# Kernel tuning notes

Measured on AMD Instinct MI355X. Metric: run time of the kernel, lower is better.

Reference implementation:

```python
import jax, jax.numpy as jnp
import numpy as np

_DN = ('NCHW', 'OIHW', 'NCHW')


def _gaussian_kernel1d(ksize, sigma):
    x = np.arange(ksize, dtype=np.float32) - ksize // 2
    g = np.exp(-x ** 2 / (2.0 * sigma ** 2))
    return (g / g.sum()).astype(np.float32)


def _nms_kernels():
    # kornia get_canny_nms_kernel: kernel k = center - neighbor at angle k*45deg (0deg = +x/right)
    k = np.zeros((8, 1, 3, 3), dtype=np.float32)
    offs = [(0, 1), (-1, 1), (-1, 0), (-1, -1), (0, -1), (1, -1), (1, 0), (1, 1)]
    for i, (dy, dx) in enumerate(offs):
        k[i, 0, 1, 1] = 1.0
        k[i, 0, 1 + dy, 1 + dx] = -1.0
    return k


def _conv(x, w, padding):
    return jax.lax.conv_general_dilated(x, w, (1, 1), padding, dimension_numbers=_DN)


def _canny_magnitude(data):
    eps = 1e-6
    x = (data + 1.0) / 2.0
    # rgb -> grayscale (kornia weights)
    rgb_w = jnp.array([0.299, 0.587, 0.114], dtype=x.dtype)
    gray = jnp.einsum('bchw,c->bhw', x, rgb_w)[:, None]  # [B,1,H,W]
    # gaussian blur 5x5, sigma=1, reflect border (kornia default), separable
    g1d = jnp.asarray(_gaussian_kernel1d(5, 1.0), dtype=x.dtype)
    p = jnp.pad(gray, ((0, 0), (0, 0), (2, 2), (2, 2)), mode='reflect')
    blurred = _conv(_conv(p, g1d.reshape(1, 1, 1, 5), 'VALID'), g1d.reshape(1, 1, 5, 1), 'VALID')
    # sobel spatial gradient (normalized=False), replicate padding
    sob_x = jnp.array([[-1., 0., 1.], [-2., 0., 2.], [-1., 0., 1.]], dtype=x.dtype)
    sob = jnp.stack([sob_x, sob_x.T])[:, None]  # [2,1,3,3]
    bp = jnp.pad(blurred, ((0, 0), (0, 0), (1, 1), (1, 1)), mode='edge')
    grads = _conv(bp, sob, 'VALID')  # [B,2,H,W]
    gx, gy = grads[:, 0:1], grads[:, 1:2]
    magnitude = jnp.sqrt(gx * gx + gy * gy + eps)  # [B,1,H,W]
    # angle rounded to nearest 45 degrees
    ang45 = jnp.round(jnp.rad2deg(jnp.arctan2(gy, gx)) / 45.0)
    # non-maximum suppression: center-minus-neighbor along 8 directions (zero pad)
    nms_k = jnp.asarray(_nms_kernels(), dtype=x.dtype)
    nms_mag = _conv(magnitude, nms_k, ((1, 1), (1, 1)))  # [B,8,H,W]
    idx_pos = ang45.astype(jnp.int32) % 8
    idx_neg = (idx_pos + 4) % 8
    sel_pos = jnp.take_along_axis(nms_mag, idx_pos, axis=1)
    sel_neg = jnp.take_along_axis(nms_mag, idx_neg, axis=1)
    is_max = jnp.minimum(sel_pos, sel_neg) > 0.0
    return magnitude * is_max


def setup_inputs() -> dict:
    key = jax.random.key(0)
    data = jax.random.normal(key, (16, 3, 512, 512), dtype=jnp.float32)
    return {'data': data}


def reference(data):
    # EdgeOperator.forward: canny((data+1)/2)[0] -> NMS'd gradient magnitude [B,1,H,W]
    return _canny_magnitude(data)
```

## Files before the change

### kernel.cpp

```cpp
#include <hip/hip_runtime.h>
#include <math.h>

#define IMH 512
#define IMW 512
#define T   32
#define GS  40

#define LG  44
#define OG  0
#define LH  40
#define OH  1760
#define LB  40
#define OB  3360
#define LM  40
#define OM  4800
#define LX  32
#define OGX 0
#define OGY 1024
#define NPOOL 6160

__device__ __forceinline__ int reflect_i(int v, int n) {
    if (v < 0) v = -v;
    if (v >= n) v = 2 * n - 2 - v;
    return v;
}
__device__ __forceinline__ int clamp_i(int v, int n) {
    return v < 0 ? 0 : (v >= n ? n - 1 : v);
}

__global__ __launch_bounds__(256)
void canny_mag_kernel(const float* __restrict__ data, float* __restrict__ out) {
    __shared__ __align__(16) float sP[NPOOL];
    const int bx0 = blockIdx.x * T;
    const int by0 = blockIdx.y * T;
    const int b   = blockIdx.z;
    const int tid = threadIdx.x;
    const bool xin = (bx0 >= 4) && (bx0 + T + 4 <= IMW);
    const bool bin = (bx0 >= 1) && (bx0 + T + 1 <= IMW) &&
                     (by0 >= 1) && (by0 + T + 1 <= IMH);

    const float w0 = 0.05448868f, w1 = 0.24420134f, w2 = 0.40261995f;
    const size_t plane = (size_t)IMH * IMW;
    const float* p0 = data + (size_t)b * 3 * plane;
    const float* p1 = p0 + plane;
    const float* p2 = p1 + plane;

    if (xin) {
        for (int idx = tid; idx < GS * 10; idx += 256) {
            int r = idx / 10, c4 = idx - r * 10;
            int ry = reflect_i(by0 - 4 + r, IMH);
            int off = ry * IMW + (bx0 - 4) + c4 * 4;
            const float4 a = *(const float4*)(p0 + off);
            const float4 g = *(const float4*)(p1 + off);
            const float4 c = *(const float4*)(p2 + off);
            float4 o;
            o.x = 0.1495f * a.x + 0.2935f * g.x + 0.057f * c.x + 0.5f;
            o.y = 0.1495f * a.y + 0.2935f * g.y + 0.057f * c.y + 0.5f;
            o.z = 0.1495f * a.z + 0.2935f * g.z + 0.057f * c.z + 0.5f;
            o.w = 0.1495f * a.w + 0.2935f * g.w + 0.057f * c.w + 0.5f;
            *(float4*)&sP[OG + r * LG + c4 * 4] = o;
        }
    } else {
        for (int idx = tid; idx < GS * GS; idx += 256) {
            int i = idx / GS, j = idx - i * GS;
            int ry = reflect_i(by0 - 4 + i, IMH);
            int rx = reflect_i(bx0 - 4 + j, IMW);
            int off = ry * IMW + rx;
            sP[OG + i * LG + j] = 0.1495f * p0[off] + 0.2935f * p1[off] + 0.057f * p2[off] + 0.5f;
        }
    }
    __syncthreads();

    if (xin) {
        for (int idx = tid; idx < GS * 9; idx += 256) {
            int i = idx / 9, gq = idx - i * 9;
            const float4 A = *(const float4*)&sP[OG + i * LG + 4 * gq];
            const float4 Bv = *(const float4*)&sP[OG + i * LG + 4 * gq + 4];
            float W0 = A.x, W1 = A.y, W2 = A.z, W3 = A.w;
            float W4 = Bv.x, W5 = Bv.y, W6 = Bv.z, W7 = Bv.w;
            float4 o;
            o.x = w0 * (W0 + W4) + w1 * (W1 + W3) + w2 * W2;
            o.y = w0 * (W1 + W5) + w1 * (W2 + W4) + w2 * W3;
            o.z = w0 * (W2 + W6) + w1 * (W3 + W5) + w2 * W4;
            o.w = w0 * (W3 + W7) + w1 * (W4 + W6) + w2 * W5;
            *(float4*)&sP[OH + i * LH + 4 * gq] = o;
        }
    } else {
        for (int idx = tid; idx < GS * 36; idx += 256) {
            int i = idx / 36, j = idx - i * 36;
            int cj = clamp_i(bx0 - 2 + j, IMW) - bx0 + 4;
            const float* gp = &sP[OG + i * LG + cj];
            sP[OH + i * LH + j] = w0 * (gp[-2] + gp[2]) + w1 * (gp[-1] + gp[1]) + w2 * gp[0];
        }
    }
    __syncthreads();

    for (int idx = tid; idx < 36 * 9; idx += 256) {
        int jy = idx / 9, gq = idx - jy * 9;
        int ci = clamp_i(by0 - 2 + jy, IMH) - by0 + 4;
        int base = OH + ci * LH + 4 * gq;
        const float4 r0 = *(const float4*)&sP[base - 2 * LH];
        const float4 r1 = *(const float4*)&sP[base - LH];
        const float4 r2 = *(const float4*)&sP[base];
        const float4 r3 = *(const float4*)&sP[base + LH];
        const float4 r4 = *(const float4*)&sP[base + 2 * LH];
        float4 o;
        o.x = w0 * (r0.x + r4.x) + w1 * (r1.x + r3.x) + w2 * r2.x;
        o.y = w0 * (r0.y + r4.y) + w1 * (r1.y + r3.y) + w2 * r2.y;
        o.z = w0 * (r0.z + r4.z) + w1 * (r1.z + r3.z) + w2 * r2.z;
        o.w = w0 * (r0.w + r4.w) + w1 * (r1.w + r3.w) + w2 * r2.w;
        *(float4*)&sP[OB + jy * LB + 4 * gq + 4] = o;
    }
    __syncthreads();

    for (int idx = tid; idx < 34 * 10; idx += 256) {
        int iy = idx / 10, gq = idx - iy * 10;
        int baseB = OB + iy * LB + 4 * gq;
        const float4 t0a = *(const float4*)&sP[baseB];
        const float4 t0b = *(const float4*)&sP[baseB + 4];
        const float4 t1a = *(const float4*)&sP[baseB + LB];
        const float4 t1b = *(const float4*)&sP[baseB + LB + 4];
        const float4 t2a = *(const float4*)&sP[baseB + 2 * LB];
        const float4 t2b = *(const float4*)&sP[baseB + 2 * LB + 4];
        float W0[8] = {t0a.x, t0a.y, t0a.z, t0a.w, t0b.x, t0b.y, t0b.z, t0b.w};
        float W1[8] = {t1a.x, t1a.y, t1a.z, t1a.w, t1b.x, t1b.y, t1b.z, t1b.w};
        float W2[8] = {t2a.x, t2a.y, t2a.z, t2a.w, t2b.x, t2b.y, t2b.z, t2b.w};
        float mg[4], gxv[4], gyv[4];
        #pragma unroll
        for (int k = 0; k < 4; ++k) {
            float a00 = W0[k + 1], a01 = W0[k + 2], a02 = W0[k + 3];
            float a10 = W1[k + 1],                  a12 = W1[k + 3];
            float a20 = W2[k + 1], a21 = W2[k + 2], a22 = W2[k + 3];
            float gx = (a02 - a00) + 2.0f * (a12 - a10) + (a22 - a20);
            float gy = (a20 - a00) + 2.0f * (a21 - a01) + (a22 - a02);
            float m = sqrtf(gx * gx + gy * gy + 1e-6f);
            if (!bin) {
                int my = by0 - 1 + iy;
                int cx = bx0 - 4 + 4 * gq + k;
                if (my < 0 || my >= IMH || cx < 0 || cx >= IMW) m = 0.0f;
            }
            mg[k] = m; gxv[k] = gx; gyv[k] = gy;
        }
        *(float4*)&sP[OM + iy * LM + 4 * gq] = make_float4(mg[0], mg[1], mg[2], mg[3]);
        if (gq >= 1 && gq <= 8 && iy >= 1 && iy <= 32) {
            int st = (iy - 1) * LX + 4 * gq - 4;
            *(float4*)&sP[OGX + st] = make_float4(gxv[0], gxv[1], gxv[2], gxv[3]);
            *(float4*)&sP[OGY + st] = make_float4(gyv[0], gyv[1], gyv[2], gyv[3]);
        }
    }
    __syncthreads();

    {
        const int ly  = tid >> 3;
        const int lx0 = (tid & 7) * 4;
        const float4 mag4 = *(const float4*)&sP[OM + (ly + 1) * LM + lx0 + 4];
        const float4 gx4  = *(const float4*)&sP[OGX + ly * LX + lx0];
        const float4 gy4  = *(const float4*)&sP[OGY + ly * LX + lx0];
        const float magv[4] = {mag4.x, mag4.y, mag4.z, mag4.w};
        const float gxv2[4] = {gx4.x, gx4.y, gx4.z, gx4.w};
        const float gyv2[4] = {gy4.x, gy4.y, gy4.z, gy4.w};
        float ov[4];
        #pragma unroll
        for (int k = 0; k < 4; ++k) {
            float gx = gxv2[k], gy = gyv2[k], mag = magv[k];
            float ax = fabsf(gx), ay = fabsf(gy);
            int dy, dx;
            if (ay <= 0.41421356237f * ax)      { dy = 0; dx = 1; }
            else if (ay >= 2.41421356237f * ax) { dy = 1; dx = 0; }
            else                                { dx = 1; dy = (gx * gy > 0.0f) ? -1 : 1; }
            float n1 = sP[OM + (ly + 1 + dy) * LM + (lx0 + k + 4 + dx)];
            float n2 = sP[OM + (ly + 1 - dy) * LM + (lx0 + k + 4 - dx)];
            ov[k] = (mag > n1 && mag > n2) ? mag : 0.0f;
        }
        float4 o4 = make_float4(ov[0], ov[1], ov[2], ov[3]);
        *(float4*)&out[(size_t)b * plane + (size_t)(by0 + ly) * IMW + (bx0 + lx0)] = o4;
    }
}

extern "C" void kernel_launch(void* const* d_in, const int* in_sizes, int n_in,
                              void* d_out, int out_size, void* d_ws, size_t ws_size,
                              hipStream_t stream) {
    const float* data = (const float*)d_in[0];
    float* out = (float*)d_out;
    int B = in_sizes[0] / (3 * IMH * IMW);
    dim3 grid(IMW / T, IMH / T, B);
    canny_mag_kernel<<<grid, dim3(256, 1, 1), 0, stream>>>(data, out);
}
```

Measured before the change: 104.5 us.

## Fuse grayscale with horizontal blur and alias shared buffers to cut LDS

```diff
diff --git a/kernel.cpp b/kernel.cpp
--- a/kernel.cpp
+++ b/kernel.cpp
@@ -4,20 +4,14 @@
 #define IMH 512
 #define IMW 512
 #define T   32
-#define GS  40
 
-#define LG  44
-#define OG  0
-#define LH  40
-#define OH  1760
+#define LH  36
+#define OH  0
+#define LM  40
+#define OM  0
 #define LB  40
-#define OB  3360
-#define LM  40
-#define OM  4800
-#define LX  32
-#define OGX 0
-#define OGY 1024
-#define NPOOL 6160
+#define OB  1440
+#define NPOOL 3200
 
 __device__ __forceinline__ int reflect_i(int v, int n) {
     if (v < 0) v = -v;
@@ -28,7 +22,7 @@
     return v < 0 ? 0 : (v >= n ? n - 1 : v);
 }
 
-__global__ __launch_bounds__(256)
+__global__ __launch_bounds__(256, 8)
 void canny_mag_kernel(const float* __restrict__ data, float* __restrict__ out) {
     __shared__ __align__(16) float sP[NPOOL];
     const int bx0 = blockIdx.x * T;
@@ -46,50 +40,45 @@
     const float* p2 = p1 + plane;
 
     if (xin) {
-        for (int idx = tid; idx < GS * 10; idx += 256) {
-            int r = idx / 10, c4 = idx - r * 10;
-            int ry = reflect_i(by0 - 4 + r, IMH);
-            int off = ry * IMW + (bx0 - 4) + c4 * 4;
-            const float4 a = *(const float4*)(p0 + off);
-            const float4 g = *(const float4*)(p1 + off);
-            const float4 c = *(const float4*)(p2 + off);
+        for (int idx = tid; idx < 40 * 9; idx += 256) {
+            int i = idx / 9, gq = idx - i * 9;
+            int ry = reflect_i(by0 - 4 + i, IMH);
+            int off = ry * IMW + (bx0 - 4) + 4 * gq;
+            const float4 a0 = *(const float4*)(p0 + off);
+            const float4 a1 = *(const float4*)(p0 + off + 4);
+            const float4 g0 = *(const float4*)(p1 + off);
+            const float4 g1 = *(const float4*)(p1 + off + 4);
+            const float4 c0 = *(const float4*)(p2 + off);
+            const float4 c1 = *(const float4*)(p2 + off + 4);
+            float w[8];
+            w[0] = 0.1495f * a0.x + 0.2935f * g0.x + 0.057f * c0.x + 0.5f;
+            w[1] = 0.1495f * a0.y + 0.2935f * g0.y + 0.057f * c0.y + 0.5f;
+            w[2] = 0.1495f * a0.z + 0.2935f * g0.z + 0.057f * c0.z + 0.5f;
+            w[3] = 0.1495f * a0.w + 0.2935f * g0.w + 0.057f * c0.w + 0.5f;
+            w[4] = 0.1495f * a1.x + 0.2935f * g1.x + 0.057f * c1.x + 0.5f;
+            w[5] = 0.1495f * a1.y + 0.2935f * g1.y + 0.057f * c1.y + 0.5f;
+            w[6] = 0.1495f * a1.z + 0.2935f * g1.z + 0.057f * c1.z + 0.5f;
+            w[7] = 0.1495f * a1.w + 0.2935f * g1.w + 0.057f * c1.w + 0.5f;
             float4 o;
-            o.x = 0.1495f * a.x + 0.2935f * g.x + 0.057f * c.x + 0.5f;
-            o.y = 0.1495f * a.y + 0.2935f * g.y + 0.057f * c.y + 0.5f;
-            o.z = 0.1495f * a.z + 0.2935f * g.z + 0.057f * c.z + 0.5f;
-            o.w = 0.1495f * a.w + 0.2935f * g.w + 0.057f * c.w + 0.5f;
-            *(float4*)&sP[OG + r * LG + c4 * 4] = o;
+            o.x = w0 * (w[0] + w[4]) + w1 * (w[1] + w[3]) + w2 * w[2];
+            o.y = w0 * (w[1] + w[5]) + w1 * (w[2] + w[4]) + w2 * w[3];
+            o.z = w0 * (w[2] + w[6]) + w1 * (w[3] + w[5]) + w2 * w[4];
+            o.w = w0 * (w[3] + w[7]) + w1 * (w[4] + w[6]) + w2 * w[5];
+            *(float4*)&sP[OH + i * LH + 4 * gq] = o;
         }
     } else {
-        for (int idx = tid; idx < GS * GS; idx += 256) {
-            int i = idx / GS, j = idx - i * GS;
+        for (int idx = tid; idx < 40 * 40; idx += 256) {
+            int i = idx / 40, j = idx - i * 40;
             int ry = reflect_i(by0 - 4 + i, IMH);
             int rx = reflect_i(bx0 - 4 + j, IMW);
             int off = ry * IMW + rx;
-            sP[OG + i * LG + j] = 0.1495f * p0[off] + 0.2935f * p1[off] + 0.057f * p2[off] + 0.5f;
+            sP[OB + i * 40 + j] = 0.1495f * p0[off] + 0.2935f * p1[off] + 0.057f * p2[off] + 0.5f;
         }
-    }
-    __syncthreads();
-
-    if (xin) {
-        for (int idx = tid; idx < GS * 9; idx += 256) {
-            int i = idx / 9, gq = idx - i * 9;
-            const float4 A = *(const float4*)&sP[OG + i * LG + 4 * gq];
-            const float4 Bv = *(const float4*)&sP[OG + i * LG + 4 * gq + 4];
-            float W0 = A.x, W1 = A.y, W2 = A.z, W3 = A.w;
-            float W4 = Bv.x, W5 = Bv.y, W6 = Bv.z, W7 = Bv.w;
-            float4 o;
-            o.x = w0 * (W0 + W4) + w1 * (W1 + W3) + w2 * W2;
-            o.y = w0 * (W1 + W5) + w1 * (W2 + W4) + w2 * W3;
-            o.z = w0 * (W2 + W6) + w1 * (W3 + W5) + w2 * W4;
-            o.w = w0 * (W3 + W7) + w1 * (W4 + W6) + w2 * W5;
-            *(float4*)&sP[OH + i * LH + 4 * gq] = o;
-        }
-    } else {
-        for (int idx = tid; idx < GS * 36; idx += 256) {
+        __syncthreads();
+        for (int idx = tid; idx < 40 * 36; idx += 256) {
             int i = idx / 36, j = idx - i * 36;
             int cj = clamp_i(bx0 - 2 + j, IMW) - bx0 + 4;
-            const float* gp = &sP[OG + i * LG + cj];
+            const float* gp = &sP[OB + i * 40 + cj];
             sP[OH + i * LH + j] = w0 * (gp[-2] + gp[2]) + w1 * (gp[-1] + gp[1]) + w2 * gp[0];
         }
     }
@@ -125,7 +114,7 @@
         float W0[8] = {t0a.x, t0a.y, t0a.z, t0a.w, t0b.x, t0b.y, t0b.z, t0b.w};
         float W1[8] = {t1a.x, t1a.y, t1a.z, t1a.w, t1b.x, t1b.y, t1b.z, t1b.w};
         float W2[8] = {t2a.x, t2a.y, t2a.z, t2a.w, t2b.x, t2b.y, t2b.z, t2b.w};
-        float mg[4], gxv[4], gyv[4];
+        float mg[4];
         #pragma unroll
         for (int k = 0; k < 4; ++k) {
             float a00 = W0[k + 1], a01 = W0[k + 2], a02 = W0[k + 3];
@@ -139,30 +128,35 @@
                 int cx = bx0 - 4 + 4 * gq + k;
                 if (my < 0 || my >= IMH || cx < 0 || cx >= IMW) m = 0.0f;
             }
-            mg[k] = m; gxv[k] = gx; gyv[k] = gy;
+            mg[k] = m;
         }
         *(float4*)&sP[OM + iy * LM + 4 * gq] = make_float4(mg[0], mg[1], mg[2], mg[3]);
-        if (gq >= 1 && gq <= 8 && iy >= 1 && iy <= 32) {
-            int st = (iy - 1) * LX + 4 * gq - 4;
-            *(float4*)&sP[OGX + st] = make_float4(gxv[0], gxv[1], gxv[2], gxv[3]);
-            *(float4*)&sP[OGY + st] = make_float4(gyv[0], gyv[1], gyv[2], gyv[3]);
-        }
     }
     __syncthreads();
 
     {
         const int ly  = tid >> 3;
         const int lx0 = (tid & 7) * 4;
-        const float4 mag4 = *(const float4*)&sP[OM + (ly + 1) * LM + lx0 + 4];
-        const float4 gx4  = *(const float4*)&sP[OGX + ly * LX + lx0];
-        const float4 gy4  = *(const float4*)&sP[OGY + ly * LX + lx0];
-        const float magv[4] = {mag4.x, mag4.y, mag4.z, mag4.w};
-        const float gxv2[4] = {gx4.x, gx4.y, gx4.z, gx4.w};
-        const float gyv2[4] = {gy4.x, gy4.y, gy4.z, gy4.w};
+        const float4 m4 = *(const float4*)&sP[OM + (ly + 1) * LM + lx0 + 4];
+        const int bB = OB + (ly + 1) * LB + lx0 + 4;
+        const float4 u0a = *(const float4*)&sP[bB];
+        const float4 u0b = *(const float4*)&sP[bB + 4];
+        const float4 u1a = *(const float4*)&sP[bB + LB];
+        const float4 u1b = *(const float4*)&sP[bB + LB + 4];
+        const float4 u2a = *(const float4*)&sP[bB + 2 * LB];
+        const float4 u2b = *(const float4*)&sP[bB + 2 * LB + 4];
+        float U0[8] = {u0a.x, u0a.y, u0a.z, u0a.w, u0b.x, u0b.y, u0b.z, u0b.w};
+        float U1[8] = {u1a.x, u1a.y, u1a.z, u1a.w, u1b.x, u1b.y, u1b.z, u1b.w};
+        float U2[8] = {u2a.x, u2a.y, u2a.z, u2a.w, u2b.x, u2b.y, u2b.z, u2b.w};
+        const float magv[4] = {m4.x, m4.y, m4.z, m4.w};
         float ov[4];
         #pragma unroll
         for (int k = 0; k < 4; ++k) {
-            float gx = gxv2[k], gy = gyv2[k], mag = magv[k];
+            float a00 = U0[k + 1], a01 = U0[k + 2], a02 = U0[k + 3];
+            float a10 = U1[k + 1],                  a12 = U1[k + 3];
+            float a20 = U2[k + 1], a21 = U2[k + 2], a22 = U2[k + 3];
+            float gx = (a02 - a00) + 2.0f * (a12 - a10) + (a22 - a20);
+            float gy = (a20 - a00) + 2.0f * (a21 - a01) + (a22 - a02);
             float ax = fabsf(gx), ay = fabsf(gy);
             int dy, dx;
             if (ay <= 0.41421356237f * ax)      { dy = 0; dx = 1; }
@@ -170,6 +164,7 @@
             else                                { dx = 1; dy = (gx * gy > 0.0f) ? -1 : 1; }
             float n1 = sP[OM + (ly + 1 + dy) * LM + (lx0 + k + 4 + dx)];
             float n2 = sP[OM + (ly + 1 - dy) * LM + (lx0 + k + 4 - dx)];
+            float mag = magv[k];
             ov[k] = (mag > n1 && mag > n2) ? mag : 0.0f;
         }
         float4 o4 = make_float4(ov[0], ov[1], ov[2], ov[3]);
```

Result: no change. 104.0 us (-0.5%).
